# Performance work log

Measured on AMD Instinct MI355X. Metric: run time of the kernel, lower is better.

Reference implementation:

```python
import jax, jax.numpy as jnp
import numpy as np

N_NODES = 100000
N_EDGES = 1600000
IN_CH = 64
HID = 64
N_CLASSES = 10
N_GRAPHS = 64


def setup_inputs() -> dict:
    key = jax.random.key(0)
    ks = jax.random.split(key, 12)
    x = jax.random.normal(ks[0], (N_NODES, IN_CH), dtype=jnp.float32)
    edge_index = jax.random.randint(ks[1], (2, N_EDGES), 0, N_NODES, dtype=jnp.int64)
    batch = jnp.sort(jax.random.randint(ks[2], (N_NODES,), 0, N_GRAPHS, dtype=jnp.int64))

    def glorot(k, fan_in, fan_out):
        lim = jnp.sqrt(6.0 / (fan_in + fan_out))
        return jax.random.uniform(k, (fan_in, fan_out), jnp.float32, -lim, lim)

    W1 = glorot(ks[3], IN_CH, HID); b1 = jnp.zeros((HID,), jnp.float32)
    W2 = glorot(ks[4], HID, HID);   b2 = jnp.zeros((HID,), jnp.float32)
    W3 = glorot(ks[5], HID, HID);   b3 = jnp.zeros((HID,), jnp.float32)
    Wc = glorot(ks[6], HID, N_CLASSES)
    bc = jnp.zeros((N_CLASSES,), jnp.float32)
    return {"x": x, "edge_index": edge_index, "batch": batch,
            "W1": W1, "b1": b1, "W2": W2, "b2": b2, "W3": W3, "b3": b3,
            "Wc": Wc, "bc": bc}


def _gcn_conv(x, W, b, src, dst, edge_norm, self_norm):
    # x' = D^-1/2 (A+I) D^-1/2 (x W) + b  (PyG GCNConv with self-loops)
    h = x @ W                                    # [N, H] small GEMM
    msg = h[src] * edge_norm[:, None]            # [E, H] gather (memory-bound)
    agg = jax.ops.segment_sum(msg, dst, num_segments=N_NODES)  # scatter-add
    agg = agg + h * self_norm[:, None]           # self-loop contribution
    return agg + b


def reference(x, edge_index, batch, W1, b1, W2, b2, W3, b3, Wc, bc):
    src, dst = edge_index[0], edge_index[1]
    # degree on target nodes including self-loop (PyG gcn_norm)
    deg = jax.ops.segment_sum(jnp.ones((N_EDGES,), x.dtype), dst,
                              num_segments=N_NODES) + 1.0
    dinv = jnp.where(deg > 0, deg ** -0.5, 0.0)
    edge_norm = dinv[src] * dinv[dst]            # [E]
    self_norm = dinv * dinv                      # [N]

    h = jax.nn.relu(_gcn_conv(x, W1, b1, src, dst, edge_norm, self_norm))
    h = jax.nn.relu(_gcn_conv(h, W2, b2, src, dst, edge_norm, self_norm))
    h = jax.nn.relu(_gcn_conv(h, W3, b3, src, dst, edge_norm, self_norm))

    # global mean pool per graph
    sums = jax.ops.segment_sum(h, batch, num_segments=N_GRAPHS)       # [G, H]
    cnts = jax.ops.segment_sum(jnp.ones((N_NODES,), h.dtype), batch,
                               num_segments=N_GRAPHS)
    graph_emb = sums / jnp.maximum(cnts, 1.0)[:, None]
    return graph_emb @ Wc + bc                   # [G, num_classes]
```

## Files before the change

### kernel.cpp

```cpp
#include <hip/hip_runtime.h>


#define HIDDEN 64
#define BSHIFT 8
#define MAXB 512
#define BCAP 5120

typedef __attribute__((ext_vector_type(8))) short bf16x8;
typedef __attribute__((ext_vector_type(4))) float f32x4;

__device__ __forceinline__ unsigned short f32_to_bf16_rne(float f) {
    unsigned u = __float_as_uint(f);
    u += 0x7FFF + ((u >> 16) & 1);
    return (unsigned short)(u >> 16);
}
__device__ __forceinline__ float bf16_to_f32(unsigned short h) {
    return __uint_as_float((unsigned)h << 16);
}

__global__ __launch_bounds__(256) void scatter_onepass(const int* __restrict__ src,
                                                       const int* __restrict__ dst,
                                                       int* __restrict__ gCursor,
                                                       unsigned* __restrict__ rec,
                                                       int E, int perBlock) {
    __shared__ int hist[MAXB];
    __shared__ int cur[MAXB];
    for (int i = threadIdx.x; i < MAXB; i += 256) hist[i] = 0;
    __syncthreads();
    int beg = blockIdx.x * perBlock;
    int end = min(beg + perBlock, E);
    if (beg >= end) return;
    int n4 = (end - beg) >> 2;
    const int4* d4 = reinterpret_cast<const int4*>(dst + beg);
    const int4* s4 = reinterpret_cast<const int4*>(src + beg);
    for (int g = threadIdx.x; g < n4; g += 256) {
        int4 d = d4[g];
        atomicAdd(&hist[d.x >> BSHIFT], 1);
        atomicAdd(&hist[d.y >> BSHIFT], 1);
        atomicAdd(&hist[d.z >> BSHIFT], 1);
        atomicAdd(&hist[d.w >> BSHIFT], 1);
    }
    for (int e = beg + (n4 << 2) + threadIdx.x; e < end; e += 256)
        atomicAdd(&hist[dst[e] >> BSHIFT], 1);
    __syncthreads();
    for (int i = threadIdx.x; i < MAXB; i += 256)
        cur[i] = hist[i] ? (i * BCAP + atomicAdd(&gCursor[i], hist[i])) : 0;
    __syncthreads();
    for (int g = threadIdx.x; g < n4; g += 256) {
        int4 d = d4[g];
        int4 s = s4[g];
        int p;
        p = atomicAdd(&cur[d.x >> BSHIFT], 1); rec[p] = ((unsigned)s.x << 8) | (unsigned)(d.x & 255);
        p = atomicAdd(&cur[d.y >> BSHIFT], 1); rec[p] = ((unsigned)s.y << 8) | (unsigned)(d.y & 255);
        p = atomicAdd(&cur[d.z >> BSHIFT], 1); rec[p] = ((unsigned)s.z << 8) | (unsigned)(d.z & 255);
        p = atomicAdd(&cur[d.w >> BSHIFT], 1); rec[p] = ((unsigned)s.w << 8) | (unsigned)(d.w & 255);
    }
    for (int e = beg + (n4 << 2) + threadIdx.x; e < end; e += 256) {
        int d = dst[e];
        int p = atomicAdd(&cur[d >> BSHIFT], 1);
        rec[p] = ((unsigned)src[e] << 8) | (unsigned)(d & 255);
    }
}

__global__ __launch_bounds__(256) void bucket_build(const unsigned* __restrict__ rec,
                                                    const int* __restrict__ gCursor,
                                                    int* __restrict__ rowBeg,
                                                    int* __restrict__ rowEnd,
                                                    float* __restrict__ dinv,
                                                    int* __restrict__ col, int N) {
    int b = blockIdx.x;
    int base = b * BCAP, cnt = gCursor[b];
    int t = threadIdx.x;
    __shared__ int hist[256];
    __shared__ int sc[256];
    __shared__ int cur[256];
    hist[t] = 0;
    __syncthreads();
    for (int i = base + t; i < base + cnt; i += 256)
        atomicAdd(&hist[rec[i] & 255], 1);
    __syncthreads();
    int myCnt = hist[t];
    sc[t] = myCnt;
    __syncthreads();
    for (int off = 1; off < 256; off <<= 1) {
        int u = (t >= off) ? sc[t - off] : 0;
        __syncthreads();
        sc[t] += u;
        __syncthreads();
    }
    int nodeBase = base + sc[t] - myCnt;
    int node = (b << BSHIFT) + t;
    if (node < N) {
        rowBeg[node] = nodeBase;
        rowEnd[node] = nodeBase + myCnt;
        dinv[node] = rsqrtf((float)(myCnt + 1));
    }
    cur[t] = nodeBase;
    __syncthreads();
    for (int i = base + t; i < base + cnt; i += 256) {
        unsigned r = rec[i];
        int p = atomicAdd(&cur[r & 255], 1);
        col[p] = (int)(r >> 8);
    }
}

template<bool F32IN>
__global__ __launch_bounds__(256) void gemm_mfma(const void* __restrict__ Xin,
                                                 const float* __restrict__ W,
                                                 const float* __restrict__ dinv,
                                                 unsigned short* __restrict__ Hs, int N) {
    __shared__ __align__(16) unsigned short Wh_t[64][72];
    __shared__ __align__(16) unsigned short Wl_t[64][72];
    int t = threadIdx.x;
    for (int i = t; i < 4096; i += 256) {
        int k = i >> 6, c = i & 63;
        float w = W[i];
        unsigned short h = f32_to_bf16_rne(w);
        Wh_t[c][k] = h;
        Wl_t[c][k] = f32_to_bf16_rne(w - bf16_to_f32(h));
    }
    __syncthreads();
    int w = t >> 6, lane = t & 63;
    int lr = lane & 15, lk = lane >> 4;
    int rowBase = blockIdx.x * 128;
#pragma unroll
    for (int tile = 0; tile < 2; tile++) {
        int arow = rowBase + tile * 64 + w * 16 + lr;
        int rr = min(arow, N - 1);
        bf16x8 a0, a1;
        if (F32IN) {
            const float* xp = (const float*)Xin + ((size_t)rr << 6) + lk * 8;
            float4 p0 = *reinterpret_cast<const float4*>(xp);
            float4 p1 = *reinterpret_cast<const float4*>(xp + 4);
            float4 p2 = *reinterpret_cast<const float4*>(xp + 32);
            float4 p3 = *reinterpret_cast<const float4*>(xp + 36);
            a0[0] = (short)f32_to_bf16_rne(p0.x); a0[1] = (short)f32_to_bf16_rne(p0.y);
            a0[2] = (short)f32_to_bf16_rne(p0.z); a0[3] = (short)f32_to_bf16_rne(p0.w);
            a0[4] = (short)f32_to_bf16_rne(p1.x); a0[5] = (short)f32_to_bf16_rne(p1.y);
            a0[6] = (short)f32_to_bf16_rne(p1.z); a0[7] = (short)f32_to_bf16_rne(p1.w);
            a1[0] = (short)f32_to_bf16_rne(p2.x); a1[1] = (short)f32_to_bf16_rne(p2.y);
            a1[2] = (short)f32_to_bf16_rne(p2.z); a1[3] = (short)f32_to_bf16_rne(p2.w);
            a1[4] = (short)f32_to_bf16_rne(p3.x); a1[5] = (short)f32_to_bf16_rne(p3.y);
            a1[6] = (short)f32_to_bf16_rne(p3.z); a1[7] = (short)f32_to_bf16_rne(p3.w);
        } else {
            const unsigned short* xp = (const unsigned short*)Xin + ((size_t)rr << 6) + lk * 8;
            a0 = *reinterpret_cast<const bf16x8*>(xp);
            a1 = *reinterpret_cast<const bf16x8*>(xp + 32);
        }
        f32x4 zero = {0.f, 0.f, 0.f, 0.f};
        f32x4 acc[4];
        acc[0] = zero; acc[1] = zero; acc[2] = zero; acc[3] = zero;
#pragma unroll
        for (int ct = 0; ct < 4; ct++) {
            int bcol = ct * 16 + lr;
            bf16x8 bh0 = *reinterpret_cast<const bf16x8*>(&Wh_t[bcol][lk * 8]);
            bf16x8 bl0 = *reinterpret_cast<const bf16x8*>(&Wl_t[bcol][lk * 8]);
            bf16x8 bh1 = *reinterpret_cast<const bf16x8*>(&Wh_t[bcol][32 + lk * 8]);
            bf16x8 bl1 = *reinterpret_cast<const bf16x8*>(&Wl_t[bcol][32 + lk * 8]);
            acc[ct] = __builtin_amdgcn_mfma_f32_16x16x32_bf16(a0, bh0, acc[ct], 0, 0, 0);
            acc[ct] = __builtin_amdgcn_mfma_f32_16x16x32_bf16(a0, bl0, acc[ct], 0, 0, 0);
            acc[ct] = __builtin_amdgcn_mfma_f32_16x16x32_bf16(a1, bh1, acc[ct], 0, 0, 0);
            acc[ct] = __builtin_amdgcn_mfma_f32_16x16x32_bf16(a1, bl1, acc[ct], 0, 0, 0);
        }
#pragma unroll
        for (int i = 0; i < 4; i++) {
            int row = rowBase + tile * 64 + w * 16 + lk * 4 + i;
            if (row < N) {
                float dn = dinv[row];
#pragma unroll
                for (int ct = 0; ct < 4; ct++) {
                    Hs[(size_t)row * 64 + ct * 16 + lr] = f32_to_bf16_rne(dn * acc[ct][i]);
                }
            }
        }
    }
}

__global__ __launch_bounds__(256) void aggregate_kernel(const unsigned short* __restrict__ Hs,
                                                        const int* __restrict__ rowBeg,
                                                        const int* __restrict__ rowEnd,
                                                        const int* __restrict__ col,
                                                        const float* __restrict__ dinv,
                                                        const float* __restrict__ bias,
                                                        unsigned short* __restrict__ OUT, int N) {
    int node = blockIdx.x * 4 + (threadIdx.x >> 6);
    int lane = threadIdx.x & 63;
    if (node >= N) return;
    int beg = __builtin_amdgcn_readfirstlane(rowBeg[node]);
    int end = __builtin_amdgcn_readfirstlane(rowEnd[node]);
    float a0 = 0.f, a1 = 0.f, a2 = 0.f, a3 = 0.f;
    float a4 = 0.f, a5 = 0.f, a6 = 0.f, a7 = 0.f;
    int e = beg;
    if (e + 8 <= end) {
        int c0 = col[e],     c1 = col[e + 1], c2 = col[e + 2], c3 = col[e + 3];
        int c4 = col[e + 4], c5 = col[e + 5], c6 = col[e + 6], c7 = col[e + 7];
        while (true) {
            int en = e + 8;
            bool more = (en + 8 <= end);
            int n0, n1, n2, n3, n4, n5, n6, n7;
            if (more) {
                n0 = col[en];     n1 = col[en + 1]; n2 = col[en + 2]; n3 = col[en + 3];
                n4 = col[en + 4]; n5 = col[en + 5]; n6 = col[en + 6]; n7 = col[en + 7];
            }
            unsigned short v0 = Hs[(size_t)c0 * 64 + lane];
            unsigned short v1 = Hs[(size_t)c1 * 64 + lane];
            unsigned short v2 = Hs[(size_t)c2 * 64 + lane];
            unsigned short v3 = Hs[(size_t)c3 * 64 + lane];
            unsigned short v4 = Hs[(size_t)c4 * 64 + lane];
            unsigned short v5 = Hs[(size_t)c5 * 64 + lane];
            unsigned short v6 = Hs[(size_t)c6 * 64 + lane];
            unsigned short v7 = Hs[(size_t)c7 * 64 + lane];
            a0 += bf16_to_f32(v0); a1 += bf16_to_f32(v1);
            a2 += bf16_to_f32(v2); a3 += bf16_to_f32(v3);
            a4 += bf16_to_f32(v4); a5 += bf16_to_f32(v5);
            a6 += bf16_to_f32(v6); a7 += bf16_to_f32(v7);
            e = en;
            if (!more) break;
            c0 = n0; c1 = n1; c2 = n2; c3 = n3;
            c4 = n4; c5 = n5; c6 = n6; c7 = n7;
        }
    }
    for (; e < end; e++) a0 += bf16_to_f32(Hs[(size_t)col[e] * 64 + lane]);
    float acc = ((a0 + a1) + (a2 + a3)) + ((a4 + a5) + (a6 + a7));
    acc += bf16_to_f32(Hs[(size_t)node * 64 + lane]);
    acc = fmaxf(acc * dinv[node] + bias[lane], 0.f);
    OUT[(size_t)node * 64 + lane] = f32_to_bf16_rne(acc);
}

__global__ __launch_bounds__(256) void pool_partial(const unsigned short* __restrict__ H,
                                                    const int* __restrict__ batch,
                                                    float* __restrict__ sums, int N) {
    int wid = (blockIdx.x * blockDim.x + threadIdx.x) >> 6;
    int lane = threadIdx.x & 63;
    int start = wid * 64;
    if (start >= N) return;
    int end = min(start + 64, N);
    int g = batch[start];
    float acc = 0.f;
    for (int n = start; n < end; n++) {
        int bg = batch[n];
        if (bg != g) { atomicAdd(&sums[g * 64 + lane], acc); acc = 0.f; g = bg; }
        acc += bf16_to_f32(H[(size_t)n * 64 + lane]);
    }
    atomicAdd(&sums[g * 64 + lane], acc);
}

__device__ __forceinline__ int lower_bound_dev(const int* a, int n, int key) {
    int lo = 0, hi = n;
    while (lo < hi) { int mid = (lo + hi) >> 1; if (a[mid] < key) lo = mid + 1; else hi = mid; }
    return lo;
}

__global__ void classify_kernel(const float* __restrict__ sums, const float* __restrict__ Wc,
                                const float* __restrict__ bc, const int* __restrict__ batch,
                                float* __restrict__ out, int N) {
    int t = blockIdx.x * blockDim.x + threadIdx.x;
    if (t >= 64 * 10) return;
    int g = t / 10, c = t % 10;
    float acc = 0.f;
    for (int k = 0; k < 64; k++) acc += sums[g * 64 + k] * Wc[k * 10 + c];
    int cnt = lower_bound_dev(batch, N, g + 1) - lower_bound_dev(batch, N, g);
    out[t] = acc / (float)max(cnt, 1) + bc[c];
}

extern "C" void kernel_launch(void* const* d_in, const int* in_sizes, int n_in,
                              void* d_out, int out_size, void* d_ws, size_t ws_size,
                              hipStream_t stream) {
    const float* x  = (const float*)d_in[0];
    const int* ei   = (const int*)d_in[1];
    const int* batch= (const int*)d_in[2];
    const float* W1 = (const float*)d_in[3];
    const float* b1 = (const float*)d_in[4];
    const float* W2 = (const float*)d_in[5];
    const float* b2 = (const float*)d_in[6];
    const float* W3 = (const float*)d_in[7];
    const float* b3 = (const float*)d_in[8];
    const float* Wc = (const float*)d_in[9];
    const float* bc = (const float*)d_in[10];

    int N = in_sizes[0] / HIDDEN;
    int E = in_sizes[1] / 2;
    const int* src = ei;
    const int* dst = ei + E;
    int NB = (N + 255) >> 8;

    char* ws = (char*)d_ws;
    size_t off = 0;
    auto alloc = [&](size_t bytes) { void* p = ws + off; off = (off + bytes + 255) & ~(size_t)255; return p; };
    int*   gCursor= (int*)  alloc((size_t)MAXB * 4);
    int*   rowBeg = (int*)  alloc((size_t)N * 4);
    int*   rowEnd = (int*)  alloc((size_t)N * 4);
    float* dinv   = (float*)alloc((size_t)N * 4);
    int*   col    = (int*)  alloc((size_t)NB * BCAP * 4);
    unsigned short* hb = (unsigned short*)alloc((size_t)N * HIDDEN * 2);
    unsigned short* ha = (unsigned short*)alloc((size_t)N * HIDDEN * 2);
    float* sums   = (float*)alloc(64 * 64 * 4);
    unsigned* rec = (unsigned*)alloc((size_t)NB * BCAP * 4);

    int grid = 256;
    int perBlock = (((E + grid - 1) / grid) + 3) & ~3;
    hipMemsetAsync(gCursor, 0, (size_t)MAXB * 4, stream);
    hipMemsetAsync(sums, 0, 64 * 64 * 4, stream);
    scatter_onepass<<<grid, 256, 0, stream>>>(src, dst, gCursor, rec, E, perBlock);
    bucket_build<<<NB, 256, 0, stream>>>(rec, gCursor, rowBeg, rowEnd, dinv, col, N);

    int gGemm = (N + 127) / 128;
    int gAgg  = (N + 3) / 4;
    gemm_mfma<true><<<gGemm, 256, 0, stream>>>(x, W1, dinv, hb, N);
    aggregate_kernel<<<gAgg, 256, 0, stream>>>(hb, rowBeg, rowEnd, col, dinv, b1, ha, N);
    gemm_mfma<false><<<gGemm, 256, 0, stream>>>(ha, W2, dinv, hb, N);
    aggregate_kernel<<<gAgg, 256, 0, stream>>>(hb, rowBeg, rowEnd, col, dinv, b2, ha, N);
    gemm_mfma<false><<<gGemm, 256, 0, stream>>>(ha, W3, dinv, hb, N);
    aggregate_kernel<<<gAgg, 256, 0, stream>>>(hb, rowBeg, rowEnd, col, dinv, b3, ha, N);

    pool_partial<<<(N + 255) / 256, 256, 0, stream>>>(ha, batch, sums, N);
    classify_kernel<<<1, 640, 0, stream>>>(sums, Wc, bc, batch, (float*)d_out, N);
}
```

Baseline: 269.3 us.

## Fuse mean-pool partial sums into final aggregation and merge memsets

```diff
diff --git a/kernel.cpp b/kernel.cpp
--- a/kernel.cpp
+++ b/kernel.cpp
@@ -176,73 +176,71 @@
     }
 }
 
+template<bool POOL>
 __global__ __launch_bounds__(256) void aggregate_kernel(const unsigned short* __restrict__ Hs,
                                                         const int* __restrict__ rowBeg,
                                                         const int* __restrict__ rowEnd,
                                                         const int* __restrict__ col,
                                                         const float* __restrict__ dinv,
                                                         const float* __restrict__ bias,
-                                                        unsigned short* __restrict__ OUT, int N) {
-    int node = blockIdx.x * 4 + (threadIdx.x >> 6);
+                                                        unsigned short* __restrict__ OUT,
+                                                        const int* __restrict__ batch,
+                                                        float* __restrict__ sums, int N) {
+    int wid = threadIdx.x >> 6;
+    int node = blockIdx.x * 4 + wid;
     int lane = threadIdx.x & 63;
-    if (node >= N) return;
-    int beg = __builtin_amdgcn_readfirstlane(rowBeg[node]);
-    int end = __builtin_amdgcn_readfirstlane(rowEnd[node]);
-    float a0 = 0.f, a1 = 0.f, a2 = 0.f, a3 = 0.f;
-    float a4 = 0.f, a5 = 0.f, a6 = 0.f, a7 = 0.f;
-    int e = beg;
-    if (e + 8 <= end) {
-        int c0 = col[e],     c1 = col[e + 1], c2 = col[e + 2], c3 = col[e + 3];
-        int c4 = col[e + 4], c5 = col[e + 5], c6 = col[e + 6], c7 = col[e + 7];
-        while (true) {
-            int en = e + 8;
-            bool more = (en + 8 <= end);
-            int n0, n1, n2, n3, n4, n5, n6, n7;
-            if (more) {
-                n0 = col[en];     n1 = col[en + 1]; n2 = col[en + 2]; n3 = col[en + 3];
-                n4 = col[en + 4]; n5 = col[en + 5]; n6 = col[en + 6]; n7 = col[en + 7];
-            }
-            unsigned short v0 = Hs[(size_t)c0 * 64 + lane];
-            unsigned short v1 = Hs[(size_t)c1 * 64 + lane];
-            unsigned short v2 = Hs[(size_t)c2 * 64 + lane];
-            unsigned short v3 = Hs[(size_t)c3 * 64 + lane];
-            unsigned short v4 = Hs[(size_t)c4 * 64 + lane];
-            unsigned short v5 = Hs[(size_t)c5 * 64 + lane];
-            unsigned short v6 = Hs[(size_t)c6 * 64 + lane];
-            unsigned short v7 = Hs[(size_t)c7 * 64 + lane];
+    __shared__ float red[4][64];
+    __shared__ int g4[4];
+    if (!POOL && node >= N) return;
+    float r = 0.f;
+    if (node < N) {
+        int beg = __builtin_amdgcn_readfirstlane(rowBeg[node]);
+        int end = __builtin_amdgcn_readfirstlane(rowEnd[node]);
+        float a0 = 0.f, a1 = 0.f, a2 = 0.f, a3 = 0.f;
+        float a4 = 0.f, a5 = 0.f, a6 = 0.f, a7 = 0.f;
+        int e = beg;
+        for (; e + 8 <= end; e += 8) {
+            int s0 = col[e],     s1 = col[e + 1], s2 = col[e + 2], s3 = col[e + 3];
+            int s4 = col[e + 4], s5 = col[e + 5], s6 = col[e + 6], s7 = col[e + 7];
+            unsigned short v0 = Hs[(size_t)s0 * 64 + lane];
+            unsigned short v1 = Hs[(size_t)s1 * 64 + lane];
+            unsigned short v2 = Hs[(size_t)s2 * 64 + lane];
+            unsigned short v3 = Hs[(size_t)s3 * 64 + lane];
+            unsigned short v4 = Hs[(size_t)s4 * 64 + lane];
+            unsigned short v5 = Hs[(size_t)s5 * 64 + lane];
+            unsigned short v6 = Hs[(size_t)s6 * 64 + lane];
+            unsigned short v7 = Hs[(size_t)s7 * 64 + lane];
             a0 += bf16_to_f32(v0); a1 += bf16_to_f32(v1);
             a2 += bf16_to_f32(v2); a3 += bf16_to_f32(v3);
             a4 += bf16_to_f32(v4); a5 += bf16_to_f32(v5);
             a6 += bf16_to_f32(v6); a7 += bf16_to_f32(v7);
-            e = en;
-            if (!more) break;
-            c0 = n0; c1 = n1; c2 = n2; c3 = n3;
-            c4 = n4; c5 = n5; c6 = n6; c7 = n7;
-        }
-    }
-    for (; e < end; e++) a0 += bf16_to_f32(Hs[(size_t)col[e] * 64 + lane]);
-    float acc = ((a0 + a1) + (a2 + a3)) + ((a4 + a5) + (a6 + a7));
-    acc += bf16_to_f32(Hs[(size_t)node * 64 + lane]);
-    acc = fmaxf(acc * dinv[node] + bias[lane], 0.f);
-    OUT[(size_t)node * 64 + lane] = f32_to_bf16_rne(acc);
-}
-
-__global__ __launch_bounds__(256) void pool_partial(const unsigned short* __restrict__ H,
-                                                    const int* __restrict__ batch,
-                                                    float* __restrict__ sums, int N) {
-    int wid = (blockIdx.x * blockDim.x + threadIdx.x) >> 6;
-    int lane = threadIdx.x & 63;
-    int start = wid * 64;
-    if (start >= N) return;
-    int end = min(start + 64, N);
-    int g = batch[start];
-    float acc = 0.f;
-    for (int n = start; n < end; n++) {
-        int bg = batch[n];
-        if (bg != g) { atomicAdd(&sums[g * 64 + lane], acc); acc = 0.f; g = bg; }
-        acc += bf16_to_f32(H[(size_t)n * 64 + lane]);
-    }
-    atomicAdd(&sums[g * 64 + lane], acc);
+        }
+        for (; e < end; e++) a0 += bf16_to_f32(Hs[(size_t)col[e] * 64 + lane]);
+        float acc = ((a0 + a1) + (a2 + a3)) + ((a4 + a5) + (a6 + a7));
+        acc += bf16_to_f32(Hs[(size_t)node * 64 + lane]);
+        r = fmaxf(acc * dinv[node] + bias[lane], 0.f);
+        if (!POOL) OUT[(size_t)node * 64 + lane] = f32_to_bf16_rne(r);
+    }
+    if (POOL) {
+        red[wid][lane] = r;
+        if (lane == 0) g4[wid] = (node < N) ? batch[node] : -1;
+        __syncthreads();
+        if (wid == 0) {
+            float acc2 = 0.f;
+            int curg = -2;
+#pragma unroll
+            for (int j = 0; j < 4; j++) {
+                int gj = g4[j];
+                if (gj != curg) {
+                    if (curg >= 0) atomicAdd(&sums[curg * 64 + lane], acc2);
+                    acc2 = 0.f;
+                    curg = gj;
+                }
+                if (gj >= 0) acc2 += red[j][lane];
+            }
+            if (curg >= 0) atomicAdd(&sums[curg * 64 + lane], acc2);
+        }
+    }
 }
 
 __device__ __forceinline__ int lower_bound_dev(const int* a, int n, int key) {
@@ -288,31 +286,29 @@
     size_t off = 0;
     auto alloc = [&](size_t bytes) { void* p = ws + off; off = (off + bytes + 255) & ~(size_t)255; return p; };
     int*   gCursor= (int*)  alloc((size_t)MAXB * 4);
+    float* sums   = (float*)alloc(64 * 64 * 4);
     int*   rowBeg = (int*)  alloc((size_t)N * 4);
     int*   rowEnd = (int*)  alloc((size_t)N * 4);
     float* dinv   = (float*)alloc((size_t)N * 4);
     int*   col    = (int*)  alloc((size_t)NB * BCAP * 4);
     unsigned short* hb = (unsigned short*)alloc((size_t)N * HIDDEN * 2);
     unsigned short* ha = (unsigned short*)alloc((size_t)N * HIDDEN * 2);
-    float* sums   = (float*)alloc(64 * 64 * 4);
     unsigned* rec = (unsigned*)alloc((size_t)NB * BCAP * 4);
 
     int grid = 256;
     int perBlock = (((E + grid - 1) / grid) + 3) & ~3;
-    hipMemsetAsync(gCursor, 0, (size_t)MAXB * 4, stream);
-    hipMemsetAsync(sums, 0, 64 * 64 * 4, stream);
+    hipMemsetAsync(gCursor, 0, (size_t)MAXB * 4 + 64 * 64 * 4, stream);
     scatter_onepass<<<grid, 256, 0, stream>>>(src, dst, gCursor, rec, E, perBlock);
     bucket_build<<<NB, 256, 0, stream>>>(rec, gCursor, rowBeg, rowEnd, dinv, col, N);
 
     int gGemm = (N + 127) / 128;
     int gAgg  = (N + 3) / 4;
     gemm_mfma<true><<<gGemm, 256, 0, stream>>>(x, W1, dinv, hb, N);
-    aggregate_kernel<<<gAgg, 256, 0, stream>>>(hb, rowBeg, rowEnd, col, dinv, b1, ha, N);
+    aggregate_kernel<false><<<gAgg, 256, 0, stream>>>(hb, rowBeg, rowEnd, col, dinv, b1, ha, batch, sums, N);
     gemm_mfma<false><<<gGemm, 256, 0, stream>>>(ha, W2, dinv, hb, N);
-    aggregate_kernel<<<gAgg, 256, 0, stream>>>(hb, rowBeg, rowEnd, col, dinv, b2, ha, N);
+    aggregate_kernel<false><<<gAgg, 256, 0, stream>>>(hb, rowBeg, rowEnd, col, dinv, b2, ha, batch, sums, N);
     gemm_mfma<false><<<gGemm, 256, 0, stream>>>(ha, W3, dinv, hb, N);
-    aggregate_kernel<<<gAgg, 256, 0, stream>>>(hb, rowBeg, rowEnd, col, dinv, b3, ha, N);
-
-    pool_partial<<<(N + 255) / 256, 256, 0, stream>>>(ha, batch, sums, N);
+    aggregate_kernel<true><<<gAgg, 256, 0, stream>>>(hb, rowBeg, rowEnd, col, dinv, b3, ha, batch, sums, N);
+
     classify_kernel<<<1, 640, 0, stream>>>(sums, Wc, bc, batch, (float*)d_out, N);
 }
```

Measured after the change: 267.0 us. Within noise of the previous version (-0.9%).
